# Performance work log

Measured on AMD Instinct MI355X. Metric: run time of the kernel, lower is better.

## Reference

```python
import jax, jax.numpy as jnp
import numpy as np

B, T, C = 2, 2048, 1024
NUM_HEADS = 16
HEAD_DIM = C // NUM_HEADS
TEMP = 1.0
LN_EPS = 1e-6


def setup_inputs() -> dict:
    key = jax.random.key(0)
    kx, kqw, kpw = jax.random.split(key, 3)
    x = jax.random.normal(kx, (B, T, C), dtype=jnp.float32)
    # causal mask, broadcastable to [B, H, T, T]
    mask = jnp.tril(jnp.ones((T, T), dtype=bool))[None, None, :, :]
    # LayerNorm params (flax defaults: scale=1, bias=0)
    ln_scale = jnp.ones((C,), dtype=jnp.float32)
    ln_bias = jnp.zeros((C,), dtype=jnp.float32)
    # xavier_uniform init for dense kernels, zero bias (torch_linear)
    lim_qkv = float(np.sqrt(6.0 / (C + 3 * C)))
    qkv_w = jax.random.uniform(kqw, (C, 3 * C), jnp.float32, -lim_qkv, lim_qkv)
    qkv_b = jnp.zeros((3 * C,), dtype=jnp.float32)
    lim_p = float(np.sqrt(6.0 / (C + C)))
    proj_w = jax.random.uniform(kpw, (C, C), jnp.float32, -lim_p, lim_p)
    proj_b = jnp.zeros((C,), dtype=jnp.float32)
    return {"x": x, "mask": mask, "ln_scale": ln_scale, "ln_bias": ln_bias,
            "qkv_w": qkv_w, "qkv_b": qkv_b, "proj_w": proj_w, "proj_b": proj_b}


def reference(x, mask, ln_scale, ln_bias, qkv_w, qkv_b, proj_w, proj_b):
    b, t, c = x.shape
    # LayerNorm (eps=1e-6, flax default)
    mu = jnp.mean(x, axis=-1, keepdims=True)
    var = jnp.mean(jnp.square(x - mu), axis=-1, keepdims=True)
    xn = (x - mu) * jax.lax.rsqrt(var + LN_EPS) * ln_scale + ln_bias
    # fused QKV projection
    qkv = xn @ qkv_w + qkv_b
    q, k, v = jnp.split(qkv, 3, axis=-1)
    q = q.reshape(b, t, NUM_HEADS, HEAD_DIM) / TEMP
    k = k.reshape(b, t, NUM_HEADS, HEAD_DIM)
    v = v.reshape(b, t, NUM_HEADS, HEAD_DIM)
    # scaled dot-product attention with mask (eval path: no dropout)
    q = q / jnp.sqrt(jnp.float32(HEAD_DIM)).astype(x.dtype)
    scores = jnp.einsum('bqhd,bkhd->bhqk', q, k)  # [B,H,T,T]
    big_neg = jnp.finfo(x.dtype).min
    scores = jnp.where(mask, scores, big_neg)
    attn_weights = jax.nn.softmax(scores, axis=-1).astype(x.dtype)
    out = jnp.einsum('bhqk,bkhd->bqhd', attn_weights, v).reshape(b, t, c)
    return out @ proj_w + proj_b
```

## Files before the change

### kernel.cpp

```cpp
#include <hip/hip_runtime.h>
#include <cstdint>
#include <math.h>

#define DEV __device__ __forceinline__

typedef unsigned int u32;
typedef unsigned short u16;
typedef __attribute__((ext_vector_type(4))) float f32x4;
typedef __attribute__((ext_vector_type(4))) u32 u32x4;
typedef __attribute__((ext_vector_type(2))) u32 u32x2;
typedef __attribute__((ext_vector_type(8))) __bf16 bf16x8;

static_assert(sizeof(bf16x8) == 16, "bf16x8 must be 16B");

static constexpr int Tn = 2048, Cn = 1024;
static constexpr int Mrows = 2 * Tn;
static constexpr float QSCALE2 = 0.125f * 1.44269504088896f;

DEV u16 f2bf_rne(float f) {
  u32 u = __builtin_bit_cast(u32, f);
  u32 r = u + 0x7fffu + ((u >> 16) & 1u);
  return (u16)(r >> 16);
}
DEV float bf2f(u16 h) {
  u32 u = ((u32)h) << 16;
  return __builtin_bit_cast(float, u);
}
DEV u32 pack2bf(float a, float b) {
  return (u32)f2bf_rne(a) | ((u32)f2bf_rne(b) << 16);
}
DEV u32 cvtpk(float lo, float hi) {
  u32 r;
  asm("v_cvt_pk_bf16_f32 %0, %1, %2" : "=v"(r) : "v"(lo), "v"(hi));
  return r;
}
DEV float fexp2(float x) {
#if __has_builtin(__builtin_amdgcn_exp2f)
  return __builtin_amdgcn_exp2f(x);
#else
  return exp2f(x);
#endif
}

DEV void stage16(const void* g, void* l) {
#if __has_builtin(__builtin_amdgcn_global_load_lds)
  __builtin_amdgcn_global_load_lds(
      (__attribute__((address_space(1))) u32*)(uintptr_t)g,
      (__attribute__((address_space(3))) u32*)l, 16, 0, 0);
#else
  *(u32x4*)l = *(const u32x4*)g;
#endif
}

__global__ __launch_bounds__(256) void ln_kernel(const float* __restrict__ x,
                                                 const float* __restrict__ sc,
                                                 const float* __restrict__ bi,
                                                 u16* __restrict__ xn) {
  int row = blockIdx.x;
  int t = threadIdx.x;
  const float* xr = x + (size_t)row * Cn;
  f32x4 v = *(const f32x4*)(xr + t * 4);
  float s = v.x + v.y + v.z + v.w;
  float s2 = v.x * v.x + v.y * v.y + v.z * v.z + v.w * v.w;
#pragma unroll
  for (int off = 1; off < 64; off <<= 1) {
    s += __shfl_xor(s, off);
    s2 += __shfl_xor(s2, off);
  }
  __shared__ float red[8];
  if ((t & 63) == 0) {
    red[(t >> 6) * 2] = s;
    red[(t >> 6) * 2 + 1] = s2;
  }
  __syncthreads();
  s = red[0] + red[2] + red[4] + red[6];
  s2 = red[1] + red[3] + red[5] + red[7];
  float mean = s * (1.0f / Cn);
  float var = s2 * (1.0f / Cn) - mean * mean;
  float rstd = rsqrtf(var + 1e-6f);
  f32x4 g = *(const f32x4*)(sc + t * 4);
  f32x4 b = *(const f32x4*)(bi + t * 4);
  u32 lo = pack2bf((v.x - mean) * rstd * g.x + b.x, (v.y - mean) * rstd * g.y + b.y);
  u32 hi = pack2bf((v.z - mean) * rstd * g.z + b.z, (v.w - mean) * rstd * g.w + b.w);
  u32x2 pack = {lo, hi};
  *(u32x2*)(xn + (size_t)row * Cn + t * 4) = pack;
}

__global__ __launch_bounds__(256) void transpose_cast2(const float* __restrict__ qkv_w,
                                                       u16* __restrict__ wqkv,
                                                       const float* __restrict__ proj_w,
                                                       u16* __restrict__ wproj) {
  __shared__ float tile[32][33];
  int bx = blockIdx.x;
  const float* src;
  u16* dst;
  int Cc;
  if (bx < 96) {
    src = qkv_w; dst = wqkv; Cc = 3072;
  } else {
    src = proj_w; dst = wproj; Cc = 1024; bx -= 96;
  }
  int tx = threadIdx.x, ty = threadIdx.y;
  int c0 = bx * 32, r0 = blockIdx.y * 32;
#pragma unroll
  for (int k = 0; k < 4; ++k)
    tile[ty + 8 * k][tx] = src[(size_t)(r0 + ty + 8 * k) * Cc + c0 + tx];
  __syncthreads();
#pragma unroll
  for (int k = 0; k < 4; ++k)
    dst[(size_t)(c0 + ty + 8 * k) * 1024 + r0 + tx] = f2bf_rne(tile[tx][ty + 8 * k]);
}

__global__ __launch_bounds__(256) void vt_prep(const u16* __restrict__ qkvm,
                                               u16* __restrict__ vt) {
  __shared__ u16 tile[32][33];
  int bh = blockIdx.z;
  int b = bh >> 4, h = bh & 15;
  int t0 = blockIdx.x * 32, d0 = blockIdx.y * 32;
  int tx = threadIdx.x, ty = threadIdx.y;
#pragma unroll
  for (int k = 0; k < 4; ++k)
    tile[ty + 8 * k][tx] =
        qkvm[(size_t)(b * Tn + t0 + ty + 8 * k) * 3072 + 2 * Cn + h * 64 + d0 + tx];
  __syncthreads();
#pragma unroll
  for (int k = 0; k < 4; ++k)
    vt[((size_t)bh * 64 + d0 + ty + 8 * k) * 2048 + t0 + tx] = tile[tx][ty + 8 * k];
}

template <bool OUT_F32, bool QKV_SCALE>
__global__ __launch_bounds__(256, 3) void gemm_kernel(const u16* __restrict__ A,
                                                      const u16* __restrict__ Bt,
                                                      const float* __restrict__ bias,
                                                      void* __restrict__ Cout,
                                                      int Nsz, int Ksz) {
  __shared__ u16 As[128 * 32];
  __shared__ u16 Bs[128 * 32];
  int t = threadIdx.x;
  int l = t & 63, w = t >> 6;
  int quad = l >> 4, c16 = l & 15;
  int wm = w & 1, wn = w >> 1;
  int m0 = blockIdx.y * 128, n0 = blockIdx.x * 128;

  f32x4 acc[4][4];
#pragma unroll
  for (int mt = 0; mt < 4; ++mt)
#pragma unroll
    for (int nt = 0; nt < 4; ++nt) acc[mt][nt] = (f32x4){0.f, 0.f, 0.f, 0.f};

  for (int kk = 0; kk < Ksz; kk += 32) {
#pragma unroll
    for (int i = 0; i < 2; ++i) {
      int c = t + i * 256;
      int m = c >> 2, k8 = (c & 3) ^ ((m >> 1) & 3);
      stage16(A + (size_t)(m0 + m) * Ksz + kk + k8 * 8, (char*)As + c * 16);
    }
#pragma unroll
    for (int i = 0; i < 2; ++i) {
      int c = t + i * 256;
      int n = c >> 2, k8 = (c & 3) ^ ((n >> 1) & 3);
      stage16(Bt + (size_t)(n0 + n) * Ksz + kk + k8 * 8, (char*)Bs + c * 16);
    }
    __syncthreads();
    bf16x8 af[4], bf[4];
#pragma unroll
    for (int mt = 0; mt < 4; ++mt) {
      int m = wm * 64 + mt * 16 + c16;
      int LC = m * 4 + (quad ^ ((m >> 1) & 3));
      af[mt] = *(const bf16x8*)((const char*)As + LC * 16);
    }
#pragma unroll
    for (int nt = 0; nt < 4; ++nt) {
      int n = wn * 64 + nt * 16 + c16;
      int LC = n * 4 + (quad ^ ((n >> 1) & 3));
      bf[nt] = *(const bf16x8*)((const char*)Bs + LC * 16);
    }
#pragma unroll
    for (int mt = 0; mt < 4; ++mt)
#pragma unroll
      for (int nt = 0; nt < 4; ++nt)
        acc[mt][nt] = __builtin_amdgcn_mfma_f32_16x16x32_bf16(af[mt], bf[nt],
                                                              acc[mt][nt], 0, 0, 0);
    __syncthreads();
  }
#pragma unroll
  for (int mt = 0; mt < 4; ++mt) {
    int row = m0 + wm * 64 + mt * 16 + quad * 4;
#pragma unroll
    for (int nt = 0; nt < 4; ++nt) {
      int col = n0 + wn * 64 + nt * 16 + c16;
      float bv = bias[col];
      float scale = (QKV_SCALE && col < 1024) ? QSCALE2 : 1.0f;
#pragma unroll
      for (int r = 0; r < 4; ++r) {
        float v = (acc[mt][nt][r] + bv) * scale;
        if (OUT_F32)
          ((float*)Cout)[(size_t)(row + r) * Nsz + col] = v;
        else
          ((u16*)Cout)[(size_t)(row + r) * Nsz + col] = f2bf_rne(v);
      }
    }
  }
}

__constant__ int4 chunk_tab[31] = {
    {15, 0, 6, 0},  {10, 0, 6, 15}, {5, 0, 6, -1},
    {15, 6, 5, 1},  {15, 11, 5, 2}, {14, 0, 5, 3},  {14, 5, 5, 4},
    {14, 10, 5, 5}, {13, 0, 5, 6},  {13, 5, 5, 7},  {12, 0, 5, 9},
    {10, 6, 5, 16}, {9, 0, 5, 17},  {9, 5, 5, 18},  {8, 0, 5, 19},
    {4, 0, 5, -1},
    {13, 10, 4, 8}, {12, 5, 4, 10}, {12, 9, 4, 11}, {11, 0, 4, 12},
    {11, 4, 4, 13}, {11, 8, 4, 14}, {8, 5, 4, 20},  {7, 0, 4, 21},
    {7, 4, 4, 22},  {6, 0, 4, 23},  {3, 0, 4, -1},
    {6, 4, 3, 24},  {2, 0, 3, -1},
    {1, 0, 2, -1},
    {0, 0, 1, -1}};

__constant__ int2 comb_tab[10] = {{23, 2}, {21, 2}, {19, 2}, {17, 2}, {15, 2},
                                  {12, 3}, {9, 3},  {6, 3},  {3, 3},  {0, 3}};

__global__ __launch_bounds__(256, 2) void flash_kernel(const u16* __restrict__ qkv,
                                                       const u16* __restrict__ vt,
                                                       u16* __restrict__ aout,
                                                       u16* __restrict__ Op,
                                                       float* __restrict__ ml) {
  int4 ck = chunk_tab[blockIdx.x >> 5];
  int bh = blockIdx.x & 31;
  int qt = ck.x, k0 = ck.y, nk = ck.z, slot = ck.w;
  int b = bh >> 4, h = bh & 15;
  int t = threadIdx.x, l = t & 63, w = t >> 6;
  int quad = l >> 4, c16 = l & 15;
  int q0 = qt * 128;

  __shared__ u16 Ks[2][128 * 64];
  __shared__ u16 Vs[2][64 * 128];

  bf16x8 qf[2][2];
#pragma unroll
  for (int nt = 0; nt < 2; ++nt)
#pragma unroll
    for (int ks = 0; ks < 2; ++ks)
      qf[nt][ks] = *(const bf16x8*)(qkv +
          (size_t)(b * Tn + q0 + w * 32 + nt * 16 + c16) * 3072 +
          h * 64 + ks * 32 + quad * 8);

  float mrow[2] = {-1e30f, -1e30f};
  float lrow[2] = {0.f, 0.f};
  f32x4 o[2][4];
#pragma unroll
  for (int mq = 0; mq < 2; ++mq)
#pragma unroll
    for (int dt = 0; dt < 4; ++dt) o[mq][dt] = (f32x4){0.f, 0.f, 0.f, 0.f};

  auto stageKV = [&](int buf, int kt) {
#pragma unroll
    for (int i = 0; i < 4; ++i) {
      int c = t + i * 256;
      int key = c >> 3, d8 = (c & 7) ^ (key & 7);
      stage16(qkv + (size_t)(b * Tn + kt * 128 + key) * 3072 + Cn + h * 64 + d8 * 8,
              (char*)Ks[buf] + c * 16);
    }
#pragma unroll
    for (int i = 0; i < 4; ++i) {
      int c = t + i * 256;
      int d = c >> 4, k8 = (c & 15) ^ (d & 15);
      stage16(vt + ((size_t)bh * 64 + d) * 2048 + kt * 128 + k8 * 8,
              (char*)Vs[buf] + c * 16);
    }
  };

  stageKV(0, k0);
  __syncthreads();

  for (int it = 0; it < nk; ++it) {
    int kt = k0 + it;
    if (it + 1 < nk) stageKV((it + 1) & 1, kt + 1);
    const char* Kb = (const char*)Ks[it & 1];
    const char* Vb = (const char*)Vs[it & 1];

    f32x4 s[8][2];
#pragma unroll
    for (int mt = 0; mt < 8; ++mt)
#pragma unroll
      for (int nt = 0; nt < 2; ++nt) s[mt][nt] = (f32x4){0.f, 0.f, 0.f, 0.f};
#pragma unroll
    for (int mt = 0; mt < 8; ++mt) {
#pragma unroll
      for (int ks = 0; ks < 2; ++ks) {
        int key = mt * 16 + c16;
        int d8 = ks * 4 + quad;
        int LC = key * 8 + (d8 ^ (key & 7));
        bf16x8 kf = *(const bf16x8*)(Kb + LC * 16);
#pragma unroll
        for (int nt = 0; nt < 2; ++nt)
          s[mt][nt] = __builtin_amdgcn_mfma_f32_16x16x32_bf16(kf, qf[nt][ks],
                                                              s[mt][nt], 0, 0, 0);
      }
    }
    if (kt == qt) {
#pragma unroll
      for (int mt = 0; mt < 8; ++mt)
#pragma unroll
        for (int nt = 0; nt < 2; ++nt)
#pragma unroll
          for (int r = 0; r < 4; ++r) {
            int key = kt * 128 + mt * 16 + quad * 4 + r;
            int q = q0 + w * 32 + nt * 16 + c16;
            if (key > q) s[mt][nt][r] = -1e30f;
          }
    }
    float alph[2];
    int needv[2];
#pragma unroll
    for (int nt = 0; nt < 2; ++nt) {
      float m8[8];
#pragma unroll
      for (int mt = 0; mt < 8; ++mt)
        m8[mt] = fmaxf(fmaxf(s[mt][nt][0], s[mt][nt][1]),
                       fmaxf(s[mt][nt][2], s[mt][nt][3]));
      float rm = fmaxf(fmaxf(fmaxf(m8[0], m8[1]), fmaxf(m8[2], m8[3])),
                       fmaxf(fmaxf(m8[4], m8[5]), fmaxf(m8[6], m8[7])));
      rm = fmaxf(rm, __shfl_xor(rm, 16));
      rm = fmaxf(rm, __shfl_xor(rm, 32));
      int need = __any(rm > mrow[nt] + 6.0f);
      needv[nt] = need;
      float mnew = need ? fmaxf(mrow[nt], rm) : mrow[nt];
      alph[nt] = need ? fexp2(mrow[nt] - mnew) : 1.0f;
      mrow[nt] = mnew;
      float part[8];
#pragma unroll
      for (int mt = 0; mt < 8; ++mt) {
        float e0 = fexp2(s[mt][nt][0] - mnew);
        float e1 = fexp2(s[mt][nt][1] - mnew);
        float e2 = fexp2(s[mt][nt][2] - mnew);
        float e3 = fexp2(s[mt][nt][3] - mnew);
        s[mt][nt][0] = e0; s[mt][nt][1] = e1;
        s[mt][nt][2] = e2; s[mt][nt][3] = e3;
        part[mt] = (e0 + e1) + (e2 + e3);
      }
      float rs = ((part[0] + part[1]) + (part[2] + part[3])) +
                 ((part[4] + part[5]) + (part[6] + part[7]));
      rs += __shfl_xor(rs, 16);
      rs += __shfl_xor(rs, 32);
      lrow[nt] = lrow[nt] * alph[nt] + rs;
    }
#pragma unroll
    for (int mq = 0; mq < 2; ++mq)
      if (needv[mq]) {
#pragma unroll
        for (int r = 0; r < 4; ++r) {
          float a = __shfl(alph[mq], quad * 4 + r);
#pragma unroll
          for (int dt = 0; dt < 4; ++dt) o[mq][dt][r] *= a;
        }
      }
#pragma unroll
    for (int ksq = 0; ksq < 4; ++ksq) {
      bf16x8 pa[2];
#pragma unroll
      for (int nt = 0; nt < 2; ++nt) {
        u32 A = cvtpk(s[2 * ksq][nt][0], s[2 * ksq][nt][1]);
        u32 B = cvtpk(s[2 * ksq][nt][2], s[2 * ksq][nt][3]);
        u32 C = cvtpk(s[2 * ksq + 1][nt][0], s[2 * ksq + 1][nt][1]);
        u32 D = cvtpk(s[2 * ksq + 1][nt][2], s[2 * ksq + 1][nt][3]);
        asm volatile("v_permlane32_swap_b32 %0, %1" : "+v"(A), "+v"(C));
        asm volatile("v_permlane32_swap_b32 %0, %1" : "+v"(B), "+v"(D));
        asm volatile("v_permlane16_swap_b32 %0, %1" : "+v"(A), "+v"(C));
        asm volatile("v_permlane16_swap_b32 %0, %1" : "+v"(B), "+v"(D));
        u32x4 pk = {A, B, C, D};
        pa[nt] = __builtin_bit_cast(bf16x8, pk);
      }
#pragma unroll
      for (int dt = 0; dt < 4; ++dt) {
        int d = dt * 16 + c16;
        int vc = d * 16 + ((ksq * 4 + quad) ^ (d & 15));
        bf16x8 vf = *(const bf16x8*)(Vb + vc * 16);
#pragma unroll
        for (int mq = 0; mq < 2; ++mq)
          o[mq][dt] = __builtin_amdgcn_mfma_f32_16x16x32_bf16(pa[mq], vf,
                                                              o[mq][dt], 0, 0, 0);
      }
    }
    __syncthreads();
  }

  float linv[2] = {1.0f / lrow[0], 1.0f / lrow[1]};
  if (slot < 0) {
#pragma unroll
    for (int mq = 0; mq < 2; ++mq)
#pragma unroll
      for (int r = 0; r < 4; ++r) {
        float li = __shfl(linv[mq], quad * 4 + r);
        int q = q0 + w * 32 + mq * 16 + quad * 4 + r;
#pragma unroll
        for (int dt = 0; dt < 4; ++dt)
          aout[(size_t)(b * Tn + q) * 1024 + h * 64 + dt * 16 + c16] =
              f2bf_rne(o[mq][dt][r] * li);
      }
  } else {
    int ps = slot * 32 + bh;
#pragma unroll
    for (int mq = 0; mq < 2; ++mq)
#pragma unroll
      for (int r = 0; r < 4; ++r) {
        float li = __shfl(linv[mq], quad * 4 + r);
        int qr = w * 32 + mq * 16 + quad * 4 + r;
#pragma unroll
        for (int dt = 0; dt < 4; ++dt)
          Op[((size_t)ps * 128 + qr) * 64 + dt * 16 + c16] =
              f2bf_rne(o[mq][dt][r] * li);
      }
    if (quad == 0) {
#pragma unroll
      for (int nt = 0; nt < 2; ++nt) {
        int qr = w * 32 + nt * 16 + c16;
        ml[((size_t)ps * 128 + qr) * 2] = mrow[nt];
        ml[((size_t)ps * 128 + qr) * 2 + 1] = lrow[nt];
      }
    }
  }
}

__global__ __launch_bounds__(256) void combine_kernel(const u16* __restrict__ Op,
                                                      const float* __restrict__ ml,
                                                      u16* __restrict__ aout) {
  int qt = 6 + (blockIdx.x >> 5);
  int bh = blockIdx.x & 31;
  int b = bh >> 4, h = bh & 15;
  int2 cb = comb_tab[qt - 6];
  int base = cb.x, n = cb.y;
  int d = threadIdx.x & 63, rq = threadIdx.x >> 6;
  for (int r = 0; r < 32; ++r) {
    int row = rq * 32 + r;
    float mv[3], lv[3], ov[3];
#pragma unroll
    for (int i = 0; i < 3; ++i) {
      int ps = (base + (i < n ? i : 0)) * 32 + bh;
      bool valid = i < n;
      mv[i] = valid ? ml[((size_t)ps * 128 + row) * 2] : -1e30f;
      lv[i] = valid ? ml[((size_t)ps * 128 + row) * 2 + 1] : 0.f;
      ov[i] = valid ? bf2f(Op[((size_t)ps * 128 + row) * 64 + d]) : 0.f;
    }
    float M = fmaxf(fmaxf(mv[0], mv[1]), mv[2]);
    float w0 = fexp2(mv[0] - M) * lv[0];
    float w1 = fexp2(mv[1] - M) * lv[1];
    float w2 = fexp2(mv[2] - M) * lv[2];
    float inv = 1.0f / (w0 + w1 + w2);
    aout[(size_t)(b * Tn + qt * 128 + row) * 1024 + h * 64 + d] =
        f2bf_rne((w0 * ov[0] + w1 * ov[1] + w2 * ov[2]) * inv);
  }
}

extern "C" void kernel_launch(void* const* d_in, const int* in_sizes, int n_in,
                              void* d_out, int out_size, void* d_ws, size_t ws_size,
                              hipStream_t stream) {
  const float* x = (const float*)d_in[0];
  const float* ln_s = (const float*)d_in[2];
  const float* ln_b = (const float*)d_in[3];
  const float* qkv_w = (const float*)d_in[4];
  const float* qkv_b = (const float*)d_in[5];
  const float* proj_w = (const float*)d_in[6];
  const float* proj_b = (const float*)d_in[7];
  float* out = (float*)d_out;
  char* ws = (char*)d_ws;

  u16* xn = (u16*)ws;
  u16* wqkv = (u16*)(ws + (8ull << 20));
  u16* wproj = (u16*)(ws + (14ull << 20));
  u16* qkvm = (u16*)(ws + (16ull << 20));
  u16* attn = (u16*)(ws + (40ull << 20));
  u16* vt = (u16*)(ws + (48ull << 20));
  u16* Op = (u16*)ws;
  float* ml = (float*)(ws + (13ull << 20));

  ln_kernel<<<Mrows, 256, 0, stream>>>(x, ln_s, ln_b, xn);
  transpose_cast2<<<dim3(128, 32), dim3(32, 8), 0, stream>>>(qkv_w, wqkv, proj_w,
                                                             wproj);
  gemm_kernel<false, true><<<dim3(24, 32), 256, 0, stream>>>(xn, wqkv, qkv_b, qkvm,
                                                             3072, 1024);
  vt_prep<<<dim3(64, 2, 32), dim3(32, 8), 0, stream>>>(qkvm, vt);
  flash_kernel<<<992, 256, 0, stream>>>(qkvm, vt, attn, Op, ml);
  combine_kernel<<<320, 256, 0, stream>>>(Op, ml, attn);
  gemm_kernel<true, false><<<dim3(8, 32), 256, 0, stream>>>(attn, wproj, proj_b, out,
                                                            1024, 1024);
}
```

Baseline: 237.5 us.

## Pair adjacent query tiles per 512-thread block to share K/V staging

The flash attention kernel now runs 512-thread blocks in which two 4-wave groups handle adjacent query tiles (qt and qt-1) over the same key-tile range. Each K/V tile loaded into shared memory is reused by both groups. The chunk and combine tables are rebuilt for the new split, and the grid drops from 992 to 480 blocks. The upper group idles on key tiles past its diagonal, and doubling the block size raises register and occupancy pressure.

```diff
diff --git a/kernel.cpp b/kernel.cpp
--- a/kernel.cpp
+++ b/kernel.cpp
@@ -203,32 +203,33 @@
   }
 }
 
-__constant__ int4 chunk_tab[31] = {
-    {15, 0, 6, 0},  {10, 0, 6, 15}, {5, 0, 6, -1},
-    {15, 6, 5, 1},  {15, 11, 5, 2}, {14, 0, 5, 3},  {14, 5, 5, 4},
-    {14, 10, 5, 5}, {13, 0, 5, 6},  {13, 5, 5, 7},  {12, 0, 5, 9},
-    {10, 6, 5, 16}, {9, 0, 5, 17},  {9, 5, 5, 18},  {8, 0, 5, 19},
-    {4, 0, 5, -1},
-    {13, 10, 4, 8}, {12, 5, 4, 10}, {12, 9, 4, 11}, {11, 0, 4, 12},
-    {11, 4, 4, 13}, {11, 8, 4, 14}, {8, 5, 4, 20},  {7, 0, 4, 21},
-    {7, 4, 4, 22},  {6, 0, 4, 23},  {3, 0, 4, -1},
-    {6, 4, 3, 24},  {2, 0, 3, -1},
-    {1, 0, 2, -1},
-    {0, 0, 1, -1}};
-
-__constant__ int2 comb_tab[10] = {{23, 2}, {21, 2}, {19, 2}, {17, 2}, {15, 2},
-                                  {12, 3}, {9, 3},  {6, 3},  {3, 3},  {0, 3}};
-
-__global__ __launch_bounds__(256, 2) void flash_kernel(const u16* __restrict__ qkv,
+__constant__ int4 chunk_tab[15] = {
+    {15, 0, 6, 0},  {15, 6, 5, 1},  {15, 11, 5, 2},
+    {13, 0, 7, 6},  {13, 7, 7, 7},
+    {11, 0, 4, 10}, {11, 4, 4, 11}, {11, 8, 4, 12},
+    {9, 0, 5, 16},  {9, 5, 5, 17},
+    {7, 0, 4, 20},  {7, 4, 4, 21},
+    {5, 0, 6, -1},  {3, 0, 4, -1},  {1, 0, 2, -1}};
+__constant__ int chunk_slotB[15] = {3, 4, 5, 8, 9, 13, 14, 15,
+                                    18, 19, 22, 23, -1, -1, -1};
+
+__constant__ int2 comb_tab[10] = {{22, 2}, {20, 2}, {18, 2}, {16, 2}, {13, 3},
+                                  {10, 3}, {8, 2},  {6, 2},  {3, 3},  {0, 3}};
+
+__global__ __launch_bounds__(512, 2) void flash_kernel(const u16* __restrict__ qkv,
                                                        const u16* __restrict__ vt,
                                                        u16* __restrict__ aout,
                                                        u16* __restrict__ Op,
                                                        float* __restrict__ ml) {
-  int4 ck = chunk_tab[blockIdx.x >> 5];
+  int cid = blockIdx.x >> 5;
+  int4 ck = chunk_tab[cid];
   int bh = blockIdx.x & 31;
-  int qt = ck.x, k0 = ck.y, nk = ck.z, slot = ck.w;
+  int k0 = ck.y, nk = ck.z;
   int b = bh >> 4, h = bh & 15;
   int t = threadIdx.x, l = t & 63, w = t >> 6;
+  int g = w >> 2, wl = w & 3;
+  int qt = ck.x - g;
+  int slot = g ? chunk_slotB[cid] : ck.w;
   int quad = l >> 4, c16 = l & 15;
   int q0 = qt * 128;
 
@@ -241,7 +242,7 @@
 #pragma unroll
     for (int ks = 0; ks < 2; ++ks)
       qf[nt][ks] = *(const bf16x8*)(qkv +
-          (size_t)(b * Tn + q0 + w * 32 + nt * 16 + c16) * 3072 +
+          (size_t)(b * Tn + q0 + wl * 32 + nt * 16 + c16) * 3072 +
           h * 64 + ks * 32 + quad * 8);
 
   float mrow[2] = {-1e30f, -1e30f};
@@ -254,15 +255,15 @@
 
   auto stageKV = [&](int buf, int kt) {
 #pragma unroll
-    for (int i = 0; i < 4; ++i) {
-      int c = t + i * 256;
+    for (int i = 0; i < 2; ++i) {
+      int c = t + i * 512;
       int key = c >> 3, d8 = (c & 7) ^ (key & 7);
       stage16(qkv + (size_t)(b * Tn + kt * 128 + key) * 3072 + Cn + h * 64 + d8 * 8,
               (char*)Ks[buf] + c * 16);
     }
 #pragma unroll
-    for (int i = 0; i < 4; ++i) {
-      int c = t + i * 256;
+    for (int i = 0; i < 2; ++i) {
+      int c = t + i * 512;
       int d = c >> 4, k8 = (c & 15) ^ (d & 15);
       stage16(vt + ((size_t)bh * 64 + d) * 2048 + kt * 128 + k8 * 8,
               (char*)Vs[buf] + c * 16);
@@ -275,110 +276,113 @@
   for (int it = 0; it < nk; ++it) {
     int kt = k0 + it;
     if (it + 1 < nk) stageKV((it + 1) & 1, kt + 1);
-    const char* Kb = (const char*)Ks[it & 1];
-    const char* Vb = (const char*)Vs[it & 1];
-
-    f32x4 s[8][2];
-#pragma unroll
-    for (int mt = 0; mt < 8; ++mt)
-#pragma unroll
-      for (int nt = 0; nt < 2; ++nt) s[mt][nt] = (f32x4){0.f, 0.f, 0.f, 0.f};
-#pragma unroll
-    for (int mt = 0; mt < 8; ++mt) {
-#pragma unroll
-      for (int ks = 0; ks < 2; ++ks) {
-        int key = mt * 16 + c16;
-        int d8 = ks * 4 + quad;
-        int LC = key * 8 + (d8 ^ (key & 7));
-        bf16x8 kf = *(const bf16x8*)(Kb + LC * 16);
-#pragma unroll
-        for (int nt = 0; nt < 2; ++nt)
-          s[mt][nt] = __builtin_amdgcn_mfma_f32_16x16x32_bf16(kf, qf[nt][ks],
-                                                              s[mt][nt], 0, 0, 0);
-      }
-    }
-    if (kt == qt) {
+
+    if (kt <= qt) {
+      const char* Kb = (const char*)Ks[it & 1];
+      const char* Vb = (const char*)Vs[it & 1];
+
+      f32x4 s[8][2];
 #pragma unroll
       for (int mt = 0; mt < 8; ++mt)
 #pragma unroll
-        for (int nt = 0; nt < 2; ++nt)
+        for (int nt = 0; nt < 2; ++nt) s[mt][nt] = (f32x4){0.f, 0.f, 0.f, 0.f};
+#pragma unroll
+      for (int mt = 0; mt < 8; ++mt) {
+#pragma unroll
+        for (int ks = 0; ks < 2; ++ks) {
+          int key = mt * 16 + c16;
+          int d8 = ks * 4 + quad;
+          int LC = key * 8 + (d8 ^ (key & 7));
+          bf16x8 kf = *(const bf16x8*)(Kb + LC * 16);
+#pragma unroll
+          for (int nt = 0; nt < 2; ++nt)
+            s[mt][nt] = __builtin_amdgcn_mfma_f32_16x16x32_bf16(kf, qf[nt][ks],
+                                                                s[mt][nt], 0, 0, 0);
+        }
+      }
+      if (kt == qt) {
+#pragma unroll
+        for (int mt = 0; mt < 8; ++mt)
+#pragma unroll
+          for (int nt = 0; nt < 2; ++nt)
+#pragma unroll
+            for (int r = 0; r < 4; ++r) {
+              int key = kt * 128 + mt * 16 + quad * 4 + r;
+              int q = q0 + wl * 32 + nt * 16 + c16;
+              if (key > q) s[mt][nt][r] = -1e30f;
+            }
+      }
+      float alph[2];
+      int needv[2];
+#pragma unroll
+      for (int nt = 0; nt < 2; ++nt) {
+        float m8[8];
+#pragma unroll
+        for (int mt = 0; mt < 8; ++mt)
+          m8[mt] = fmaxf(fmaxf(s[mt][nt][0], s[mt][nt][1]),
+                         fmaxf(s[mt][nt][2], s[mt][nt][3]));
+        float rm = fmaxf(fmaxf(fmaxf(m8[0], m8[1]), fmaxf(m8[2], m8[3])),
+                         fmaxf(fmaxf(m8[4], m8[5]), fmaxf(m8[6], m8[7])));
+        rm = fmaxf(rm, __shfl_xor(rm, 16));
+        rm = fmaxf(rm, __shfl_xor(rm, 32));
+        int need = __any(rm > mrow[nt] + 6.0f);
+        needv[nt] = need;
+        float mnew = need ? fmaxf(mrow[nt], rm) : mrow[nt];
+        alph[nt] = need ? fexp2(mrow[nt] - mnew) : 1.0f;
+        mrow[nt] = mnew;
+        float part[8];
+#pragma unroll
+        for (int mt = 0; mt < 8; ++mt) {
+          float e0 = fexp2(s[mt][nt][0] - mnew);
+          float e1 = fexp2(s[mt][nt][1] - mnew);
+          float e2 = fexp2(s[mt][nt][2] - mnew);
+          float e3 = fexp2(s[mt][nt][3] - mnew);
+          s[mt][nt][0] = e0; s[mt][nt][1] = e1;
+          s[mt][nt][2] = e2; s[mt][nt][3] = e3;
+          part[mt] = (e0 + e1) + (e2 + e3);
+        }
+        float rs = ((part[0] + part[1]) + (part[2] + part[3])) +
+                   ((part[4] + part[5]) + (part[6] + part[7]));
+        rs += __shfl_xor(rs, 16);
+        rs += __shfl_xor(rs, 32);
+        lrow[nt] = lrow[nt] * alph[nt] + rs;
+      }
+#pragma unroll
+      for (int mq = 0; mq < 2; ++mq)
+        if (needv[mq]) {
 #pragma unroll
           for (int r = 0; r < 4; ++r) {
-            int key = kt * 128 + mt * 16 + quad * 4 + r;
-            int q = q0 + w * 32 + nt * 16 + c16;
-            if (key > q) s[mt][nt][r] = -1e30f;
+            float a = __shfl(alph[mq], quad * 4 + r);
+#pragma unroll
+            for (int dt = 0; dt < 4; ++dt) o[mq][dt][r] *= a;
           }
-    }
-    float alph[2];
-    int needv[2];
-#pragma unroll
-    for (int nt = 0; nt < 2; ++nt) {
-      float m8[8];
-#pragma unroll
-      for (int mt = 0; mt < 8; ++mt)
-        m8[mt] = fmaxf(fmaxf(s[mt][nt][0], s[mt][nt][1]),
-                       fmaxf(s[mt][nt][2], s[mt][nt][3]));
-      float rm = fmaxf(fmaxf(fmaxf(m8[0], m8[1]), fmaxf(m8[2], m8[3])),
-                       fmaxf(fmaxf(m8[4], m8[5]), fmaxf(m8[6], m8[7])));
-      rm = fmaxf(rm, __shfl_xor(rm, 16));
-      rm = fmaxf(rm, __shfl_xor(rm, 32));
-      int need = __any(rm > mrow[nt] + 6.0f);
-      needv[nt] = need;
-      float mnew = need ? fmaxf(mrow[nt], rm) : mrow[nt];
-      alph[nt] = need ? fexp2(mrow[nt] - mnew) : 1.0f;
-      mrow[nt] = mnew;
-      float part[8];
-#pragma unroll
-      for (int mt = 0; mt < 8; ++mt) {
-        float e0 = fexp2(s[mt][nt][0] - mnew);
-        float e1 = fexp2(s[mt][nt][1] - mnew);
-        float e2 = fexp2(s[mt][nt][2] - mnew);
-        float e3 = fexp2(s[mt][nt][3] - mnew);
-        s[mt][nt][0] = e0; s[mt][nt][1] = e1;
-        s[mt][nt][2] = e2; s[mt][nt][3] = e3;
-        part[mt] = (e0 + e1) + (e2 + e3);
-      }
-      float rs = ((part[0] + part[1]) + (part[2] + part[3])) +
-                 ((part[4] + part[5]) + (part[6] + part[7]));
-      rs += __shfl_xor(rs, 16);
-      rs += __shfl_xor(rs, 32);
-      lrow[nt] = lrow[nt] * alph[nt] + rs;
-    }
-#pragma unroll
-    for (int mq = 0; mq < 2; ++mq)
-      if (needv[mq]) {
-#pragma unroll
-        for (int r = 0; r < 4; ++r) {
-          float a = __shfl(alph[mq], quad * 4 + r);
-#pragma unroll
-          for (int dt = 0; dt < 4; ++dt) o[mq][dt][r] *= a;
         }
-      }
-#pragma unroll
-    for (int ksq = 0; ksq < 4; ++ksq) {
-      bf16x8 pa[2];
-#pragma unroll
-      for (int nt = 0; nt < 2; ++nt) {
-        u32 A = cvtpk(s[2 * ksq][nt][0], s[2 * ksq][nt][1]);
-        u32 B = cvtpk(s[2 * ksq][nt][2], s[2 * ksq][nt][3]);
-        u32 C = cvtpk(s[2 * ksq + 1][nt][0], s[2 * ksq + 1][nt][1]);
-        u32 D = cvtpk(s[2 * ksq + 1][nt][2], s[2 * ksq + 1][nt][3]);
-        asm volatile("v_permlane32_swap_b32 %0, %1" : "+v"(A), "+v"(C));
-        asm volatile("v_permlane32_swap_b32 %0, %1" : "+v"(B), "+v"(D));
-        asm volatile("v_permlane16_swap_b32 %0, %1" : "+v"(A), "+v"(C));
-        asm volatile("v_permlane16_swap_b32 %0, %1" : "+v"(B), "+v"(D));
-        u32x4 pk = {A, B, C, D};
-        pa[nt] = __builtin_bit_cast(bf16x8, pk);
-      }
-#pragma unroll
-      for (int dt = 0; dt < 4; ++dt) {
-        int d = dt * 16 + c16;
-        int vc = d * 16 + ((ksq * 4 + quad) ^ (d & 15));
-        bf16x8 vf = *(const bf16x8*)(Vb + vc * 16);
-#pragma unroll
-        for (int mq = 0; mq < 2; ++mq)
-          o[mq][dt] = __builtin_amdgcn_mfma_f32_16x16x32_bf16(pa[mq], vf,
-                                                              o[mq][dt], 0, 0, 0);
+#pragma unroll
+      for (int ksq = 0; ksq < 4; ++ksq) {
+        bf16x8 pa[2];
+#pragma unroll
+        for (int nt = 0; nt < 2; ++nt) {
+          u32 A = cvtpk(s[2 * ksq][nt][0], s[2 * ksq][nt][1]);
+          u32 B = cvtpk(s[2 * ksq][nt][2], s[2 * ksq][nt][3]);
+          u32 C = cvtpk(s[2 * ksq + 1][nt][0], s[2 * ksq + 1][nt][1]);
+          u32 D = cvtpk(s[2 * ksq + 1][nt][2], s[2 * ksq + 1][nt][3]);
+          asm volatile("v_permlane32_swap_b32 %0, %1" : "+v"(A), "+v"(C));
+          asm volatile("v_permlane32_swap_b32 %0, %1" : "+v"(B), "+v"(D));
+          asm volatile("v_permlane16_swap_b32 %0, %1" : "+v"(A), "+v"(C));
+          asm volatile("v_permlane16_swap_b32 %0, %1" : "+v"(B), "+v"(D));
+          u32x4 pk = {A, B, C, D};
+          pa[nt] = __builtin_bit_cast(bf16x8, pk);
+        }
+#pragma unroll
+        for (int dt = 0; dt < 4; ++dt) {
+          int d = dt * 16 + c16;
+          int vc = d * 16 + ((ksq * 4 + quad) ^ (d & 15));
+          bf16x8 vf = *(const bf16x8*)(Vb + vc * 16);
+#pragma unroll
+          for (int mq = 0; mq < 2; ++mq)
+            o[mq][dt] = __builtin_amdgcn_mfma_f32_16x16x32_bf16(pa[mq], vf,
+                                                                o[mq][dt], 0, 0, 0);
+        }
       }
     }
     __syncthreads();
@@ -391,7 +395,7 @@
 #pragma unroll
       for (int r = 0; r < 4; ++r) {
         float li = __shfl(linv[mq], quad * 4 + r);
-        int q = q0 + w * 32 + mq * 16 + quad * 4 + r;
+        int q = q0 + wl * 32 + mq * 16 + quad * 4 + r;
 #pragma unroll
         for (int dt = 0; dt < 4; ++dt)
           aout[(size_t)(b * Tn + q) * 1024 + h * 64 + dt * 16 + c16] =
@@ -404,7 +408,7 @@
 #pragma unroll
       for (int r = 0; r < 4; ++r) {
         float li = __shfl(linv[mq], quad * 4 + r);
-        int qr = w * 32 + mq * 16 + quad * 4 + r;
+        int qr = wl * 32 + mq * 16 + quad * 4 + r;
 #pragma unroll
         for (int dt = 0; dt < 4; ++dt)
           Op[((size_t)ps * 128 + qr) * 64 + dt * 16 + c16] =
@@ -413,7 +417,7 @@
     if (quad == 0) {
 #pragma unroll
       for (int nt = 0; nt < 2; ++nt) {
-        int qr = w * 32 + nt * 16 + c16;
+        int qr = wl * 32 + nt * 16 + c16;
         ml[((size_t)ps * 128 + qr) * 2] = mrow[nt];
         ml[((size_t)ps * 128 + qr) * 2 + 1] = lrow[nt];
       }
@@ -471,7 +475,7 @@
   u16* attn = (u16*)(ws + (40ull << 20));
   u16* vt = (u16*)(ws + (48ull << 20));
   u16* Op = (u16*)ws;
-  float* ml = (float*)(ws + (13ull << 20));
+  float* ml = (float*)(ws + (12ull << 20));
 
   ln_kernel<<<Mrows, 256, 0, stream>>>(x, ln_s, ln_b, xn);
   transpose_cast2<<<dim3(128, 32), dim3(32, 8), 0, stream>>>(qkv_w, wqkv, proj_w,
@@ -479,7 +483,7 @@
   gemm_kernel<false, true><<<dim3(24, 32), 256, 0, stream>>>(xn, wqkv, qkv_b, qkvm,
                                                              3072, 1024);
   vt_prep<<<dim3(64, 2, 32), dim3(32, 8), 0, stream>>>(qkvm, vt);
-  flash_kernel<<<992, 256, 0, stream>>>(qkvm, vt, attn, Op, ml);
+  flash_kernel<<<480, 512, 0, stream>>>(qkvm, vt, attn, Op, ml);
   combine_kernel<<<320, 256, 0, stream>>>(Op, ml, attn);
   gemm_kernel<true, false><<<dim3(8, 32), 256, 0, stream>>>(attn, wproj, proj_b, out,
                                                             1024, 1024);
```

New measurement: 243.3 us. +2.4%, slower.
